# Performance work log

Hardware: AMD Instinct MI355X
Metric: run time of the kernel (lower is better)

Reference implementation:

```python
import jax, jax.numpy as jnp
import numpy as np

PROP_TIME = 3
# (top,bottom),(left,right) zero-pad widths for the 8 neighbor shifts,
# matching torch ZeroPad2d((left,right,top,bottom)) in the original module.
PADS = [((0, 2), (0, 2)), ((0, 2), (1, 1)), ((0, 2), (2, 0)),
        ((1, 1), (0, 2)),                   ((1, 1), (2, 0)),
        ((2, 0), (0, 2)), ((2, 0), (1, 1)), ((2, 0), (2, 0))]


def _pad8(x, axis):
    """Pad last two dims 8 ways, stack the copies on `axis`."""
    lead = [(0, 0)] * (x.ndim - 2)
    return jnp.stack([jnp.pad(x, lead + [tb, lr]) for (tb, lr) in PADS], axis=axis)


def _affinity_norm(g):
    # g: [N, 8, H, W] -> gate_wb [N, 8, H+2, W+2], gate_sum [N, H, W]
    gw = jnp.stack([jnp.pad(g[:, k], [(0, 0), PADS[k][0], PADS[k][1]])
                    for k in range(8)], axis=1)
    abs_w = jnp.sum(jnp.abs(gw), axis=1, keepdims=True)
    gw = gw / abs_w
    gsum = jnp.sum(gw, axis=1)[:, 1:-1, 1:-1]
    return gw, gsum


def _propagate_once(gw, gsum, blur):
    # gw: [N,8,H+2,W+2], gsum: [N,H,W], blur: [N,B,H,W]
    nb = _pad8(blur, axis=1)                                # [N,8,B,H+2,W+2]
    ws = jnp.sum(gw[:, :, None] * nb, axis=1)[:, :, 1:-1, 1:-1]  # [N,B,H,W]
    return (1.0 - gsum[:, None]) * blur + ws


def _forward(guidance, blur, prop_time):
    # guidance: [24, X, Y, Z], blur: [B, X, Y, Z]
    gwx, gsx = _affinity_norm(jnp.transpose(guidance[0:8],   (3, 0, 1, 2)))  # [Z,8,X,Y]
    gwy, gsy = _affinity_norm(jnp.transpose(guidance[8:16],  (2, 0, 1, 3)))  # [Y,8,X,Z]
    gwz, gsz = _affinity_norm(jnp.transpose(guidance[16:24], (1, 0, 2, 3)))  # [X,8,Y,Z]
    r = blur
    for _ in range(prop_time):
        r = jnp.transpose(_propagate_once(gwx, gsx, jnp.transpose(r, (3, 0, 1, 2))), (1, 2, 3, 0))
        r = jnp.transpose(_propagate_once(gwy, gsy, jnp.transpose(r, (2, 0, 1, 3))), (1, 2, 0, 3))
        r = jnp.transpose(_propagate_once(gwz, gsz, jnp.transpose(r, (1, 0, 2, 3))), (1, 0, 2, 3))
    return r


def setup_inputs() -> dict:
    key = jax.random.key(0)
    k1, k2 = jax.random.split(key)
    guidance = jax.random.normal(k1, (24, 256, 256, 32), dtype=jnp.float32)
    blur = jax.random.normal(k2, (1, 256, 256, 32), dtype=jnp.float32)
    return {"guidance": guidance, "blur": blur}


def reference(guidance, blur):
    return _forward(guidance, blur, PROP_TIME)
```

## Files before the change

### kernel.cpp

```cpp
#include <hip/hip_runtime.h>
#include <hip/hip_fp16.h>


constexpr int X = 256, Y = 256, Z = 32;
constexpr int NV = X * Y * Z;
constexpr int YZ = Y * Z;
constexpr int NG = NV / 4;
constexpr int GEND = 24 * NV;

__device__ __forceinline__ int iclamp(int v, int lo, int hi) {
    return min(max(v, lo), hi);
}

struct alignas(16) H8 { __half2 h[4]; };

template <int DIR>
__device__ __forceinline__ void wgroup(int f0, const float* __restrict__ g,
                                       H8* __restrict__ wd) {
    constexpr int d1[8] = {1, 1, 1, 0, 0, -1, -1, -1};
    constexpr int d2[8] = {1, 0, -1, 1, -1, 1, 0, -1};
    const int z = f0 & 31, y = (f0 >> 5) & 255, x = f0 >> 13;
    const int gb0 = DIR * 8 * NV;

    float G[8][4];

    if (DIR == 0) {
#pragma unroll
        for (int k = 0; k < 8; ++k) {
            const int a = x + d1[k], b = y + d2[k];
            const bool valid = ((unsigned)a < 256u) & ((unsigned)b < 256u);
            const int ofs = f0 + d1[k] * YZ + d2[k] * Z;
            float4 gv = *(const float4*)(g + iclamp(gb0 + k * NV + ofs, 0, GEND - 4));
            if (!valid) { gv.x = 0.f; gv.y = 0.f; gv.z = 0.f; gv.w = 0.f; }
            G[k][0] = gv.x; G[k][1] = gv.y; G[k][2] = gv.z; G[k][3] = gv.w;
        }
    } else {
        const int s1 = (DIR == 1) ? YZ : Z;
        const int c1 = (DIR == 1) ? x : y;
        const bool zlo = (z > 0), zhi = (z < Z - 4);
#pragma unroll
        for (int k = 0; k < 8; ++k) {
            const bool vrow = (unsigned)(c1 + d1[k]) < 256u;
            const int gb = gb0 + k * NV + f0 + d1[k] * s1;
            float4 gv = *(const float4*)(g + iclamp(gb, 0, GEND - 4));
            if (!vrow) { gv.x = 0.f; gv.y = 0.f; gv.z = 0.f; gv.w = 0.f; }
            if (d2[k] == 1) {
                float ge = g[iclamp(gb + 4, 0, GEND - 1)];
                ge = (vrow && zhi) ? ge : 0.f;
                G[k][0] = gv.y; G[k][1] = gv.z; G[k][2] = gv.w; G[k][3] = ge;
            } else if (d2[k] == -1) {
                float ge = g[iclamp(gb - 1, 0, GEND - 1)];
                ge = (vrow && zlo) ? ge : 0.f;
                G[k][0] = ge; G[k][1] = gv.x; G[k][2] = gv.y; G[k][3] = gv.z;
            } else {
                G[k][0] = gv.x; G[k][1] = gv.y; G[k][2] = gv.z; G[k][3] = gv.w;
            }
        }
    }

#pragma unroll
    for (int i = 0; i < 4; ++i) {
        float asum = 0.f;
#pragma unroll
        for (int k = 0; k < 8; ++k) asum += fabsf(G[k][i]);
        const float winv = __builtin_amdgcn_rcpf(asum);
        H8 rec;
#pragma unroll
        for (int p = 0; p < 4; ++p)
            rec.h[p] = __floats2half2_rn(G[2 * p][i] * winv, G[2 * p + 1][i] * winv);
        wd[f0 + i] = rec;
    }
}

__global__ __launch_bounds__(256) void make_w(const float* __restrict__ g,
                                              H8* __restrict__ wd) {
    const int b = blockIdx.x;
    const int dir = b >> 11;
    const int f0 = ((b & 2047) * 256 + threadIdx.x) << 2;
    if (dir == 0)      wgroup<0>(f0, g, wd);
    else if (dir == 1) wgroup<1>(f0, g, wd + NV);
    else               wgroup<2>(f0, g, wd + 2 * NV);
}

template <int DIR>
__global__ __launch_bounds__(256) void step_w(const H8* __restrict__ w,
                                              const float* __restrict__ rin,
                                              float* __restrict__ rout) {
    constexpr int d1[8] = {1, 1, 1, 0, 0, -1, -1, -1};
    constexpr int d2[8] = {1, 0, -1, 1, -1, 1, 0, -1};
    const int t  = blockIdx.x * 256 + threadIdx.x;
    const int f0 = t << 2;

    H8 wv[4];
#pragma unroll
    for (int i = 0; i < 4; ++i) wv[i] = w[f0 + i];
    float W[4][8];
#pragma unroll
    for (int i = 0; i < 4; ++i)
#pragma unroll
        for (int p = 0; p < 4; ++p) {
            const float2 f = __half22float2(wv[i].h[p]);
            W[i][2 * p] = f.x; W[i][2 * p + 1] = f.y;
        }

    float4 rc;
    float D[8][4];

    if (DIR == 0) {
        rc = *(const float4*)(rin + f0);
#pragma unroll
        for (int k = 0; k < 8; ++k) {
            const int ofs = iclamp(f0 + d1[k] * YZ + d2[k] * Z, 0, NV - 4);
            const float4 rv = *(const float4*)(rin + ofs);
            D[k][0] = rv.x - rc.x; D[k][1] = rv.y - rc.y;
            D[k][2] = rv.z - rc.z; D[k][3] = rv.w - rc.w;
        }
    } else {
        const int s1 = (DIR == 1) ? YZ : Z;
        float4 rv[3]; float rl[3], rr[3];
#pragma unroll
        for (int j = 0; j < 3; ++j) {
            const int ro = f0 + (1 - j) * s1;
            rv[j] = *(const float4*)(rin + iclamp(ro, 0, NV - 4));
            rl[j] = rin[iclamp(ro - 1, 0, NV - 1)];
            rr[j] = rin[iclamp(ro + 4, 0, NV - 1)];
        }
        rc = rv[1];
#pragma unroll
        for (int k = 0; k < 8; ++k) {
            const int j = 1 - d1[k];
            float4 rk;
            if (d2[k] == 1)       rk = make_float4(rv[j].y, rv[j].z, rv[j].w, rr[j]);
            else if (d2[k] == -1) rk = make_float4(rl[j], rv[j].x, rv[j].y, rv[j].z);
            else                  rk = rv[j];
            D[k][0] = rk.x - rc.x; D[k][1] = rk.y - rc.y;
            D[k][2] = rk.z - rc.z; D[k][3] = rk.w - rc.w;
        }
    }

    float o[4] = {rc.x, rc.y, rc.z, rc.w};
#pragma unroll
    for (int i = 0; i < 4; ++i)
#pragma unroll
        for (int k = 0; k < 8; ++k) o[i] = fmaf(W[i][k], D[k][i], o[i]);
    *(float4*)(rout + f0) = make_float4(o[0], o[1], o[2], o[3]);
}

template <int DIR>
__global__ __launch_bounds__(256) void prop_step(const float* __restrict__ g,
                                                 const float* __restrict__ rin,
                                                 float* __restrict__ rout) {
    constexpr int d1[8] = {1, 1, 1, 0, 0, -1, -1, -1};
    constexpr int d2[8] = {1, 0, -1, 1, -1, 1, 0, -1};
    const int t = blockIdx.x * 256 + threadIdx.x;
    const int f0 = t << 2;
    const int z = f0 & 31, y = (f0 >> 5) & 255, x = f0 >> 13;
    const int gb0 = DIR * 8 * NV;

    float as[4] = {0, 0, 0, 0}, ac[4] = {0, 0, 0, 0};
    float4 rc;

    if (DIR == 0) {
        rc = *(const float4*)(rin + f0);
#pragma unroll
        for (int k = 0; k < 8; ++k) {
            const int a = x + d1[k], b = y + d2[k];
            const bool valid = ((unsigned)a < 256u) & ((unsigned)b < 256u);
            const int ofs = f0 + d1[k] * YZ + d2[k] * Z;
            const float4 rv = *(const float4*)(rin + iclamp(ofs, 0, NV - 4));
            float4 gv = *(const float4*)(g + iclamp(gb0 + k * NV + ofs, 0, GEND - 4));
            if (!valid) { gv.x = 0.f; gv.y = 0.f; gv.z = 0.f; gv.w = 0.f; }
            as[0] += fabsf(gv.x); as[1] += fabsf(gv.y);
            as[2] += fabsf(gv.z); as[3] += fabsf(gv.w);
            ac[0] = fmaf(gv.x, rv.x - rc.x, ac[0]); ac[1] = fmaf(gv.y, rv.y - rc.y, ac[1]);
            ac[2] = fmaf(gv.z, rv.z - rc.z, ac[2]); ac[3] = fmaf(gv.w, rv.w - rc.w, ac[3]);
        }
    } else {
        const int s1 = (DIR == 1) ? YZ : Z;
        const int c1 = (DIR == 1) ? x : y;
        float4 rv[3]; float rl[3], rr[3];
#pragma unroll
        for (int j = 0; j < 3; ++j) {
            const int ro = f0 + (1 - j) * s1;
            rv[j] = *(const float4*)(rin + iclamp(ro, 0, NV - 4));
            rl[j] = rin[iclamp(ro - 1, 0, NV - 1)];
            rr[j] = rin[iclamp(ro + 4, 0, NV - 1)];
        }
        rc = rv[1];
        const bool zlo = (z > 0), zhi = (z < Z - 4);
#pragma unroll
        for (int k = 0; k < 8; ++k) {
            const int j = 1 - d1[k];
            const bool vrow = (unsigned)(c1 + d1[k]) < 256u;
            const int gb = gb0 + k * NV + f0 + d1[k] * s1;
            float4 gv = *(const float4*)(g + iclamp(gb, 0, GEND - 4));
            if (!vrow) { gv.x = 0.f; gv.y = 0.f; gv.z = 0.f; gv.w = 0.f; }
            float4 gk, rk;
            if (d2[k] == 1) {
                float ge = g[iclamp(gb + 4, 0, GEND - 1)];
                ge = (vrow && zhi) ? ge : 0.f;
                gk = make_float4(gv.y, gv.z, gv.w, ge);
                rk = make_float4(rv[j].y, rv[j].z, rv[j].w, rr[j]);
            } else if (d2[k] == -1) {
                float ge = g[iclamp(gb - 1, 0, GEND - 1)];
                ge = (vrow && zlo) ? ge : 0.f;
                gk = make_float4(ge, gv.x, gv.y, gv.z);
                rk = make_float4(rl[j], rv[j].x, rv[j].y, rv[j].z);
            } else {
                gk = gv; rk = rv[j];
            }
            as[0] += fabsf(gk.x); as[1] += fabsf(gk.y);
            as[2] += fabsf(gk.z); as[3] += fabsf(gk.w);
            ac[0] = fmaf(gk.x, rk.x - rc.x, ac[0]); ac[1] = fmaf(gk.y, rk.y - rc.y, ac[1]);
            ac[2] = fmaf(gk.z, rk.z - rc.z, ac[2]); ac[3] = fmaf(gk.w, rk.w - rc.w, ac[3]);
        }
    }

    float4 o;
    o.x = rc.x + ac[0] * __builtin_amdgcn_rcpf(as[0]);
    o.y = rc.y + ac[1] * __builtin_amdgcn_rcpf(as[1]);
    o.z = rc.z + ac[2] * __builtin_amdgcn_rcpf(as[2]);
    o.w = rc.w + ac[3] * __builtin_amdgcn_rcpf(as[3]);
    *(float4*)(rout + f0) = o;
}

extern "C" void kernel_launch(void* const* d_in, const int* in_sizes, int n_in,
                              void* d_out, int out_size, void* d_ws, size_t ws_size,
                              hipStream_t stream) {
    const float* g    = (const float*)d_in[0];
    const float* blur = (const float*)d_in[1];
    float* out = (float*)d_out;

    const size_t WBYTES = (size_t)3 * NV * sizeof(H8);
    const size_t NEED   = WBYTES + (size_t)NV * sizeof(float);
    const dim3 block(256), sgrid(NG / 256);

    if (ws_size >= NEED) {
        H8*    wd   = (H8*)d_ws;
        float* bufA = (float*)((char*)d_ws + WBYTES);

        make_w<<<dim3(3 * NG / 256), block, 0, stream>>>(g, wd);

        const float* src = blur;
        for (int step = 0; step < 9; ++step) {
            float* dst = (step & 1) ? bufA : out;
            const H8* w = wd + (size_t)(step % 3) * NV;
            switch (step % 3) {
                case 0: step_w<0><<<sgrid, block, 0, stream>>>(w, src, dst); break;
                case 1: step_w<1><<<sgrid, block, 0, stream>>>(w, src, dst); break;
                case 2: step_w<2><<<sgrid, block, 0, stream>>>(w, src, dst); break;
            }
            src = dst;
        }
    } else {
        float* ws = (float*)d_ws;
        const float* src = blur;
        for (int step = 0; step < 9; ++step) {
            float* dst = (step & 1) ? ws : out;
            switch (step % 3) {
                case 0: prop_step<0><<<sgrid, block, 0, stream>>>(g, src, dst); break;
                case 1: prop_step<1><<<sgrid, block, 0, stream>>>(g, src, dst); break;
                case 2: prop_step<2><<<sgrid, block, 0, stream>>>(g, src, dst); break;
            }
            src = dst;
        }
    }
}
```

Measured before the change: 390.7 us.

## Fuse three directional propagation steps into one LDS-tiled kernel per iteration

```diff
diff --git a/kernel.cpp b/kernel.cpp
--- a/kernel.cpp
+++ b/kernel.cpp
@@ -2,21 +2,27 @@
 #include <hip/hip_fp16.h>
 
 
-constexpr int X = 256, Y = 256, Z = 32;
-constexpr int NV = X * Y * Z;
-constexpr int YZ = Y * Z;
+constexpr int NV = 256 * 256 * 32;
+constexpr int YZ = 256 * 32;
 constexpr int NG = NV / 4;
 constexpr int GEND = 24 * NV;
 
+constexpr int TXB = 8, TYB = 16;
+constexpr int RX = 12, RY = 20;
+constexpr int NCOL = RX * RY;
+constexpr int CSTR = 33;
+constexpr int LOFF = 16;
+constexpr int LSZ = NCOL * CSTR + 2 * LOFF;
+
+struct alignas(16) H8 { __half2 h[4]; };
+
 __device__ __forceinline__ int iclamp(int v, int lo, int hi) {
     return min(max(v, lo), hi);
 }
 
-struct alignas(16) H8 { __half2 h[4]; };
-
 template <int DIR>
-__device__ __forceinline__ void wgroup(int f0, const float* __restrict__ g,
-                                       H8* __restrict__ wd) {
+__device__ __forceinline__ void wgroup_t(int f0, const float* __restrict__ g,
+                                         H8* __restrict__ wt) {
     constexpr int d1[8] = {1, 1, 1, 0, 0, -1, -1, -1};
     constexpr int d2[8] = {1, 0, -1, 1, -1, 1, 0, -1};
     const int z = f0 & 31, y = (f0 >> 5) & 255, x = f0 >> 13;
@@ -29,15 +35,15 @@
         for (int k = 0; k < 8; ++k) {
             const int a = x + d1[k], b = y + d2[k];
             const bool valid = ((unsigned)a < 256u) & ((unsigned)b < 256u);
-            const int ofs = f0 + d1[k] * YZ + d2[k] * Z;
+            const int ofs = f0 + d1[k] * YZ + d2[k] * 32;
             float4 gv = *(const float4*)(g + iclamp(gb0 + k * NV + ofs, 0, GEND - 4));
             if (!valid) { gv.x = 0.f; gv.y = 0.f; gv.z = 0.f; gv.w = 0.f; }
             G[k][0] = gv.x; G[k][1] = gv.y; G[k][2] = gv.z; G[k][3] = gv.w;
         }
     } else {
-        const int s1 = (DIR == 1) ? YZ : Z;
+        const int s1 = (DIR == 1) ? YZ : 32;
         const int c1 = (DIR == 1) ? x : y;
-        const bool zlo = (z > 0), zhi = (z < Z - 4);
+        const bool zlo = (z > 0), zhi = (z < 28);
 #pragma unroll
         for (int k = 0; k < 8; ++k) {
             const bool vrow = (unsigned)(c1 + d1[k]) < 256u;
@@ -68,82 +74,108 @@
 #pragma unroll
         for (int p = 0; p < 4; ++p)
             rec.h[p] = __floats2half2_rn(G[2 * p][i] * winv, G[2 * p + 1][i] * winv);
-        wd[f0 + i] = rec;
+        const int zz = (f0 + i) & 31;
+        wt[((DIR * 32 + zz) << 16) + (x << 8) + y] = rec;
     }
 }
 
 __global__ __launch_bounds__(256) void make_w(const float* __restrict__ g,
-                                              H8* __restrict__ wd) {
+                                              H8* __restrict__ wt) {
     const int b = blockIdx.x;
     const int dir = b >> 11;
     const int f0 = ((b & 2047) * 256 + threadIdx.x) << 2;
-    if (dir == 0)      wgroup<0>(f0, g, wd);
-    else if (dir == 1) wgroup<1>(f0, g, wd + NV);
-    else               wgroup<2>(f0, g, wd + 2 * NV);
-}
-
-template <int DIR>
-__global__ __launch_bounds__(256) void step_w(const H8* __restrict__ w,
-                                              const float* __restrict__ rin,
-                                              float* __restrict__ rout) {
-    constexpr int d1[8] = {1, 1, 1, 0, 0, -1, -1, -1};
-    constexpr int d2[8] = {1, 0, -1, 1, -1, 1, 0, -1};
-    const int t  = blockIdx.x * 256 + threadIdx.x;
-    const int f0 = t << 2;
-
-    H8 wv[4];
-#pragma unroll
-    for (int i = 0; i < 4; ++i) wv[i] = w[f0 + i];
-    float W[4][8];
-#pragma unroll
-    for (int i = 0; i < 4; ++i)
-#pragma unroll
-        for (int p = 0; p < 4; ++p) {
-            const float2 f = __half22float2(wv[i].h[p]);
-            W[i][2 * p] = f.x; W[i][2 * p + 1] = f.y;
-        }
-
-    float4 rc;
-    float D[8][4];
-
-    if (DIR == 0) {
-        rc = *(const float4*)(rin + f0);
-#pragma unroll
-        for (int k = 0; k < 8; ++k) {
-            const int ofs = iclamp(f0 + d1[k] * YZ + d2[k] * Z, 0, NV - 4);
-            const float4 rv = *(const float4*)(rin + ofs);
-            D[k][0] = rv.x - rc.x; D[k][1] = rv.y - rc.y;
-            D[k][2] = rv.z - rc.z; D[k][3] = rv.w - rc.w;
-        }
-    } else {
-        const int s1 = (DIR == 1) ? YZ : Z;
-        float4 rv[3]; float rl[3], rr[3];
-#pragma unroll
-        for (int j = 0; j < 3; ++j) {
-            const int ro = f0 + (1 - j) * s1;
-            rv[j] = *(const float4*)(rin + iclamp(ro, 0, NV - 4));
-            rl[j] = rin[iclamp(ro - 1, 0, NV - 1)];
-            rr[j] = rin[iclamp(ro + 4, 0, NV - 1)];
-        }
-        rc = rv[1];
-#pragma unroll
-        for (int k = 0; k < 8; ++k) {
-            const int j = 1 - d1[k];
-            float4 rk;
-            if (d2[k] == 1)       rk = make_float4(rv[j].y, rv[j].z, rv[j].w, rr[j]);
-            else if (d2[k] == -1) rk = make_float4(rl[j], rv[j].x, rv[j].y, rv[j].z);
-            else                  rk = rv[j];
-            D[k][0] = rk.x - rc.x; D[k][1] = rk.y - rc.y;
-            D[k][2] = rk.z - rc.z; D[k][3] = rk.w - rc.w;
-        }
-    }
-
-    float o[4] = {rc.x, rc.y, rc.z, rc.w};
-#pragma unroll
-    for (int i = 0; i < 4; ++i)
-#pragma unroll
-        for (int k = 0; k < 8; ++k) o[i] = fmaf(W[i][k], D[k][i], o[i]);
-    *(float4*)(rout + f0) = make_float4(o[0], o[1], o[2], o[3]);
+    if (dir == 0)      wgroup_t<0>(f0, g, wt);
+    else if (dir == 1) wgroup_t<1>(f0, g, wt);
+    else               wgroup_t<2>(f0, g, wt);
+}
+
+template <int DIR, bool STORE>
+__device__ __forceinline__ void fstep(const H8* __restrict__ wt,
+                                      const float* __restrict__ src,
+                                      float* __restrict__ dst,
+                                      float* __restrict__ gq,
+                                      int cb, int gxc, int gyc, bool in) {
+    if (!in) return;
+    const int wb = ((DIR * 32) << 16) + (gxc << 8) + gyc;
+#pragma unroll 16
+    for (int z = 0; z < 32; ++z) {
+        const H8 wr = wt[wb + (z << 16)];
+        float w[8]; float2 f;
+        f = __half22float2(wr.h[0]); w[0] = f.x; w[1] = f.y;
+        f = __half22float2(wr.h[1]); w[2] = f.x; w[3] = f.y;
+        f = __half22float2(wr.h[2]); w[4] = f.x; w[5] = f.y;
+        f = __half22float2(wr.h[3]); w[6] = f.x; w[7] = f.y;
+        const float rc = src[cb + z];
+        float a = rc;
+        if (DIR == 0) {
+            a = fmaf(w[0], src[cb + z + (RY + 1) * CSTR] - rc, a);
+            a = fmaf(w[1], src[cb + z +  RY      * CSTR] - rc, a);
+            a = fmaf(w[2], src[cb + z + (RY - 1) * CSTR] - rc, a);
+            a = fmaf(w[3], src[cb + z +            CSTR] - rc, a);
+            a = fmaf(w[4], src[cb + z -            CSTR] - rc, a);
+            a = fmaf(w[5], src[cb + z - (RY - 1) * CSTR] - rc, a);
+            a = fmaf(w[6], src[cb + z -  RY      * CSTR] - rc, a);
+            a = fmaf(w[7], src[cb + z - (RY + 1) * CSTR] - rc, a);
+        } else if (DIR == 1) {
+            a = fmaf(w[0], src[cb + z + 1 + RY * CSTR] - rc, a);
+            a = fmaf(w[1], src[cb + z     + RY * CSTR] - rc, a);
+            a = fmaf(w[2], src[cb + z - 1 + RY * CSTR] - rc, a);
+            a = fmaf(w[3], src[cb + z + 1] - rc, a);
+            a = fmaf(w[4], src[cb + z - 1] - rc, a);
+            a = fmaf(w[5], src[cb + z + 1 - RY * CSTR] - rc, a);
+            a = fmaf(w[6], src[cb + z     - RY * CSTR] - rc, a);
+            a = fmaf(w[7], src[cb + z - 1 - RY * CSTR] - rc, a);
+        } else {
+            a = fmaf(w[0], src[cb + z + 1 + CSTR] - rc, a);
+            a = fmaf(w[1], src[cb + z     + CSTR] - rc, a);
+            a = fmaf(w[2], src[cb + z - 1 + CSTR] - rc, a);
+            a = fmaf(w[3], src[cb + z + 1] - rc, a);
+            a = fmaf(w[4], src[cb + z - 1] - rc, a);
+            a = fmaf(w[5], src[cb + z + 1 - CSTR] - rc, a);
+            a = fmaf(w[6], src[cb + z     - CSTR] - rc, a);
+            a = fmaf(w[7], src[cb + z - 1 - CSTR] - rc, a);
+        }
+        if (STORE) gq[z] = a;
+        else       dst[cb + z] = a;
+    }
+}
+
+__global__ __launch_bounds__(256) void iter3(const H8* __restrict__ wt,
+                                             const float* __restrict__ rin,
+                                             float* __restrict__ rout) {
+    __shared__ float A[LSZ];
+    __shared__ float B[LSZ];
+    const int t  = threadIdx.x;
+    const int bx = blockIdx.x & 31, by = blockIdx.x >> 5;
+    const bool act = t < NCOL;
+    const int rx = t / RY, ry = t - rx * RY;
+    const int gx = bx * TXB - 2 + rx, gy = by * TYB - 2 + ry;
+    const int gxc = iclamp(gx, 0, 255), gyc = iclamp(gy, 0, 255);
+    const int cb = t * CSTR + LOFF;
+
+    for (int i = t; i < LSZ; i += 256) { A[i] = 0.f; B[i] = 0.f; }
+    __syncthreads();
+    if (act) {
+        const float* p = rin + ((gxc << 8) + gyc) * 32;
+#pragma unroll
+        for (int j = 0; j < 8; ++j) {
+            const float4 v = *(const float4*)(p + 4 * j);
+            A[cb + 4 * j]     = v.x; A[cb + 4 * j + 1] = v.y;
+            A[cb + 4 * j + 2] = v.z; A[cb + 4 * j + 3] = v.w;
+        }
+    }
+    __syncthreads();
+
+    const bool in0 = act && rx >= 1 && rx <= RX - 2 && ry >= 1 && ry <= RY - 2;
+    const bool in1 = act && rx >= 2 && rx <= RX - 3 && ry >= 1 && ry <= RY - 2;
+    const bool in2 = act && rx >= 2 && rx <= RX - 3 && ry >= 2 && ry <= RY - 3;
+
+    fstep<0, false>(wt, A, B, nullptr, cb, gxc, gyc, in0);
+    __syncthreads();
+    fstep<1, false>(wt, B, A, nullptr, cb, gxc, gyc, in1);
+    __syncthreads();
+    float* gq = rout + ((gx << 8) + gy) * 32;
+    fstep<2, true>(wt, A, nullptr, gq, cb, gxc, gyc, in2);
 }
 
 template <int DIR>
@@ -166,7 +198,7 @@
         for (int k = 0; k < 8; ++k) {
             const int a = x + d1[k], b = y + d2[k];
             const bool valid = ((unsigned)a < 256u) & ((unsigned)b < 256u);
-            const int ofs = f0 + d1[k] * YZ + d2[k] * Z;
+            const int ofs = f0 + d1[k] * YZ + d2[k] * 32;
             const float4 rv = *(const float4*)(rin + iclamp(ofs, 0, NV - 4));
             float4 gv = *(const float4*)(g + iclamp(gb0 + k * NV + ofs, 0, GEND - 4));
             if (!valid) { gv.x = 0.f; gv.y = 0.f; gv.z = 0.f; gv.w = 0.f; }
@@ -176,7 +208,7 @@
             ac[2] = fmaf(gv.z, rv.z - rc.z, ac[2]); ac[3] = fmaf(gv.w, rv.w - rc.w, ac[3]);
         }
     } else {
-        const int s1 = (DIR == 1) ? YZ : Z;
+        const int s1 = (DIR == 1) ? YZ : 32;
         const int c1 = (DIR == 1) ? x : y;
         float4 rv[3]; float rl[3], rr[3];
 #pragma unroll
@@ -187,7 +219,7 @@
             rr[j] = rin[iclamp(ro + 4, 0, NV - 1)];
         }
         rc = rv[1];
-        const bool zlo = (z > 0), zhi = (z < Z - 4);
+        const bool zlo = (z > 0), zhi = (z < 28);
 #pragma unroll
         for (int k = 0; k < 8; ++k) {
             const int j = 1 - d1[k];
@@ -232,28 +264,20 @@
     float* out = (float*)d_out;
 
     const size_t WBYTES = (size_t)3 * NV * sizeof(H8);
-    const size_t NEED   = WBYTES + (size_t)NV * sizeof(float);
-    const dim3 block(256), sgrid(NG / 256);
+    const size_t NEED   = WBYTES + (size_t)2 * NV * sizeof(float);
 
     if (ws_size >= NEED) {
-        H8*    wd   = (H8*)d_ws;
+        H8*    wt   = (H8*)d_ws;
         float* bufA = (float*)((char*)d_ws + WBYTES);
-
-        make_w<<<dim3(3 * NG / 256), block, 0, stream>>>(g, wd);
-
-        const float* src = blur;
-        for (int step = 0; step < 9; ++step) {
-            float* dst = (step & 1) ? bufA : out;
-            const H8* w = wd + (size_t)(step % 3) * NV;
-            switch (step % 3) {
-                case 0: step_w<0><<<sgrid, block, 0, stream>>>(w, src, dst); break;
-                case 1: step_w<1><<<sgrid, block, 0, stream>>>(w, src, dst); break;
-                case 2: step_w<2><<<sgrid, block, 0, stream>>>(w, src, dst); break;
-            }
-            src = dst;
-        }
+        float* bufB = bufA + NV;
+
+        make_w<<<dim3(3 * NG / 256), dim3(256), 0, stream>>>(g, wt);
+        iter3<<<dim3(512), dim3(256), 0, stream>>>(wt, blur, bufA);
+        iter3<<<dim3(512), dim3(256), 0, stream>>>(wt, bufA, bufB);
+        iter3<<<dim3(512), dim3(256), 0, stream>>>(wt, bufB, out);
     } else {
         float* ws = (float*)d_ws;
+        const dim3 block(256), sgrid(NG / 256);
         const float* src = blur;
         for (int step = 0; step < 9; ++step) {
             float* dst = (step & 1) ? ws : out;
```

Result: faster. 357.7 us (-8.4%).
